# Performance work log

Measured on AMD Instinct MI355X. Metric: run time of the kernel, lower is better.

## Reference

```python
import jax, jax.numpy as jnp
import numpy as np

N = 50000   # nodes
E = 800000  # edges (before self loops)
D = 128     # hidden_channels (= input_dim here)
G = 64      # graphs in batch
NEG_SLOPE = 0.2


def setup_inputs() -> dict:
    key = jax.random.key(0)
    ks = jax.random.split(key, 16)
    s = 1.0 / np.sqrt(D)
    inp = {
        "x": jax.random.normal(ks[0], (N, D), jnp.float32),
        "edge_index": jax.random.randint(ks[1], (2, E), 0, N, dtype=jnp.int32),
        "batch": jnp.sort(jax.random.randint(ks[2], (N,), 0, G, dtype=jnp.int32)),
        "lin_in_w": jax.random.normal(ks[3], (D, D), jnp.float32) * s,
        "lin_in_b": jnp.zeros((D,), jnp.float32),
        "w1": jax.random.normal(ks[4], (D, D), jnp.float32) * s,
        "asrc1": jax.random.normal(ks[5], (D,), jnp.float32) * s,
        "adst1": jax.random.normal(ks[6], (D,), jnp.float32) * s,
        "b1": jnp.zeros((D,), jnp.float32),
        "w2": jax.random.normal(ks[7], (D, D), jnp.float32) * s,
        "asrc2": jax.random.normal(ks[8], (D,), jnp.float32) * s,
        "adst2": jax.random.normal(ks[9], (D,), jnp.float32) * s,
        "b2": jnp.zeros((D,), jnp.float32),
        "out_w": jax.random.normal(ks[10], (D, 1), jnp.float32) * s,
        "out_b": jnp.zeros((1,), jnp.float32),
    }
    return inp


def gat_conv(h_in, src, dst, W, a_src, a_dst, b):
    # h: [N, D] projected features (heads=1, concat irrelevant)
    h = h_in @ W
    alpha_s = (h * a_src).sum(-1)  # [N]
    alpha_d = (h * a_dst).sum(-1)  # [N]
    e = jax.nn.leaky_relu(alpha_s[src] + alpha_d[dst], NEG_SLOPE)  # [E+N]
    # segment softmax over destination nodes
    m = jax.ops.segment_max(e, dst, num_segments=N)
    e = jnp.exp(e - m[dst])
    denom = jax.ops.segment_sum(e, dst, num_segments=N)
    alpha = e / denom[dst]
    out = jax.ops.segment_sum(alpha[:, None] * h[src], dst, num_segments=N)
    return out + b


def reference(x, edge_index, batch, lin_in_w, lin_in_b,
              w1, asrc1, adst1, b1, w2, asrc2, adst2, b2, out_w, out_b):
    loops = jnp.arange(N, dtype=edge_index.dtype)
    src = jnp.concatenate([edge_index[0], loops])  # add_self_loops=True
    dst = jnp.concatenate([edge_index[1], loops])
    h = x @ lin_in_w + lin_in_b
    h = jax.nn.relu(gat_conv(h, src, dst, w1, asrc1, adst1, b1))
    h = jax.nn.relu(gat_conv(h, src, dst, w2, asrc2, adst2, b2))
    # global mean pool over graphs
    cnt = jax.ops.segment_sum(jnp.ones((N,), h.dtype), batch, num_segments=G)
    pooled = jax.ops.segment_sum(h, batch, num_segments=G) / cnt[:, None]
    return pooled @ out_w + out_b
```

## Files before the change

### kernel.cpp

```cpp
#include <hip/hip_runtime.h>
#include <hip/hip_bf16.h>

#define NEG_SLOPE 0.2f
#define BSHIFT 8
#define MAXBUCK 256
#define ECAP 8192
#define LDA 136

typedef __attribute__((ext_vector_type(8))) short bfrag;
typedef __attribute__((ext_vector_type(4))) float ffrag;

static __device__ __forceinline__ float b2f(unsigned short u){
  return __uint_as_float(((unsigned int)u) << 16);
}
static __device__ __forceinline__ unsigned short f2b16(float f){
  unsigned int u = __float_as_uint(f);
  return (unsigned short)((u + 0x7fffu + ((u >> 16) & 1u)) >> 16);
}
static __device__ __forceinline__ unsigned int pack_bf2(float a, float b){
  return (unsigned int)f2b16(a) | ((unsigned int)f2b16(b) << 16);
}

__global__ __launch_bounds__(256) void k_setup(const float* __restrict__ lin_w,
    const float* __restrict__ lin_b, const float* __restrict__ w1,
    const float* __restrict__ w2, unsigned short* __restrict__ Wtc,
    float* __restrict__ bc, unsigned short* __restrict__ Wt2,
    const int* __restrict__ batch, int* __restrict__ bcur,
    int* __restrict__ gs, int* __restrict__ ge, int n){
  __shared__ float Wl[64 * 128];
  __shared__ float Al[32 * 128];
  const int t = threadIdx.x;
  if(blockIdx.x >= 6){
    int i = (blockIdx.x - 6) * 256 + t;
    if(i < MAXBUCK) bcur[i] = 0;
    if(i < n){
      int g = batch[i];
      if(i == 0){
        gs[g] = 0;
      } else {
        int gp = batch[i - 1];
        if(gp != g){ gs[g] = i; ge[gp] = i; }
      }
      if(i == n - 1) ge[g] = n;
    }
    return;
  }
  if(blockIdx.x == 4){
    if(t < 128){
      float s = 0.f;
      for(int k = 0; k < 128; k++) s += lin_b[k] * w1[k * 128 + t];
      bc[t] = s;
    }
    return;
  }
  if(blockIdx.x == 5){
    #pragma unroll
    for(int i = 0; i < 16; i++){
      int idx = t + i * 256;
      int k = idx >> 5, n0 = (idx & 31) * 4;
      float4 v = ((const float4*)w2)[idx];
      Wt2[(n0+0) * 128 + k] = f2b16(v.x);
      Wt2[(n0+1) * 128 + k] = f2b16(v.y);
      Wt2[(n0+2) * 128 + k] = f2b16(v.z);
      Wt2[(n0+3) * 128 + k] = f2b16(v.w);
    }
    return;
  }
  const int row0 = blockIdx.x * 32;
  #pragma unroll
  for(int i = 0; i < 8; i++){
    int idx = t + i * 256;
    int r = idx >> 6, kk = idx & 63;
    ((float2*)Al)[r * 64 + kk] = ((const float2*)lin_w)[(size_t)(row0 + r) * 64 + kk];
  }
  const int c0 = (t & 31) * 4;
  const int rb = (t >> 5) * 4;
  float acc[4][4] = {};
  const float4* W4 = (const float4*)w1;
  #pragma unroll
  for(int h = 0; h < 2; h++){
    if(h) __syncthreads();
    #pragma unroll
    for(int i = 0; i < 8; i++) ((float4*)Wl)[t + i * 256] = W4[h * 2048 + t + i * 256];
    __syncthreads();
    const int kb = h * 64;
    #pragma unroll 8
    for(int k = 0; k < 64; k++){
      float4 wv = *(const float4*)&Wl[k * 128 + c0];
      float a0 = Al[(rb+0)*128 + kb + k];
      float a1 = Al[(rb+1)*128 + kb + k];
      float a2 = Al[(rb+2)*128 + kb + k];
      float a3 = Al[(rb+3)*128 + kb + k];
      acc[0][0] += a0*wv.x; acc[0][1] += a0*wv.y; acc[0][2] += a0*wv.z; acc[0][3] += a0*wv.w;
      acc[1][0] += a1*wv.x; acc[1][1] += a1*wv.y; acc[1][2] += a1*wv.z; acc[1][3] += a1*wv.w;
      acc[2][0] += a2*wv.x; acc[2][1] += a2*wv.y; acc[2][2] += a2*wv.z; acc[2][3] += a2*wv.w;
      acc[3][0] += a3*wv.x; acc[3][1] += a3*wv.y; acc[3][2] += a3*wv.z; acc[3][3] += a3*wv.w;
    }
  }
  #pragma unroll
  for(int j = 0; j < 4; j++){
    int rg = row0 + rb + j;
    Wtc[(c0+0) * 128 + rg] = f2b16(acc[j][0]);
    Wtc[(c0+1) * 128 + rg] = f2b16(acc[j][1]);
    Wtc[(c0+2) * 128 + rg] = f2b16(acc[j][2]);
    Wtc[(c0+3) * 128 + rg] = f2b16(acc[j][3]);
  }
}

template<bool ABF>
__global__ __launch_bounds__(256) void k_gemm_proj(const void* __restrict__ Av,
    const unsigned short* __restrict__ W, const float* __restrict__ a_src,
    const float* __restrict__ a_dst, const float* __restrict__ bias,
    unsigned int* __restrict__ hb,
    float* __restrict__ alpha_s, float* __restrict__ alpha_d, int nrows){
  __shared__ unsigned short Wt[128 * LDA];
  __shared__ unsigned short Aw[64 * LDA];
  const int t = threadIdx.x;
  const int row0 = blockIdx.x * 64;
  {
    const uint4* Wv = (const uint4*)W;
    #pragma unroll
    for(int i = 0; i < 8; i++){
      int idx = t + i * 256;
      int nr = idx >> 4, c8 = idx & 15;
      *(uint4*)&Wt[nr * LDA + c8 * 8] = Wv[idx];
    }
  }
  if(ABF){
    #pragma unroll
    for(int i = 0; i < 8; i++){
      int idx = t + i * 256;
      int r = idx >> 5;
      int rg = row0 + r; if(rg >= nrows) rg = nrows - 1;
      uint2 v = ((const uint2*)Av)[(size_t)rg * 32 + (idx & 31)];
      unsigned int* dst = (unsigned int*)&Aw[r * LDA];
      dst[(idx & 31) * 2]     = v.x;
      dst[(idx & 31) * 2 + 1] = v.y;
    }
  } else {
    #pragma unroll
    for(int i = 0; i < 16; i++){
      int idx = t + i * 256;
      int r = idx >> 6, c2 = idx & 63;
      int rg = row0 + r; if(rg >= nrows) rg = nrows - 1;
      float2 v = ((const float2*)Av)[(size_t)rg * 64 + c2];
      ((unsigned int*)&Aw[r * LDA])[c2] = pack_bf2(v.x, v.y);
    }
  }
  __syncthreads();

  const int lane = t & 63;
  const int wv = t >> 6;
  const int quad = lane >> 4, l = lane & 15;
  const int rw = wv * 16;
  bfrag a[4];
  #pragma unroll
  for(int kk = 0; kk < 4; kk++)
    a[kk] = *(const bfrag*)&Aw[(rw + l) * LDA + kk * 32 + quad * 8];
  ffrag acc[8];
  #pragma unroll
  for(int c = 0; c < 8; c++){
    ffrag z; z[0] = 0.f; z[1] = 0.f; z[2] = 0.f; z[3] = 0.f;
    acc[c] = z;
    #pragma unroll
    for(int kk = 0; kk < 4; kk++){
      bfrag b = *(const bfrag*)&Wt[(c * 16 + l) * LDA + kk * 32 + quad * 8];
      acc[c] = __builtin_amdgcn_mfma_f32_16x16x32_bf16(a[kk], b, acc[c], 0, 0, 0);
    }
  }
  float sdot[4] = {0.f,0.f,0.f,0.f}, ddot[4] = {0.f,0.f,0.f,0.f};
  #pragma unroll
  for(int c = 0; c < 8; c++){
    int col = c * 16 + l;
    float bv = bias ? bias[col] : 0.f;
    float as_ = a_src[col], ad_ = a_dst[col];
    #pragma unroll
    for(int r = 0; r < 4; r++){
      float v = acc[c][r] + bv;
      acc[c][r] = v;
      sdot[r] += v * as_;
      ddot[r] += v * ad_;
    }
  }
  #pragma unroll
  for(int r = 0; r < 4; r++){
    #pragma unroll
    for(int o = 1; o < 16; o <<= 1){
      sdot[r] += __shfl_xor(sdot[r], o);
      ddot[r] += __shfl_xor(ddot[r], o);
    }
  }
  if(l == 0){
    #pragma unroll
    for(int r = 0; r < 4; r++){
      int R = row0 + rw + quad * 4 + r;
      if(R < nrows){ alpha_s[R] = sdot[r]; alpha_d[R] = ddot[r]; }
    }
  }
  __syncthreads();
  unsigned short* ost = (unsigned short*)Aw;
  #pragma unroll
  for(int c = 0; c < 8; c++){
    int col = c * 16 + l;
    #pragma unroll
    for(int r = 0; r < 4; r++)
      ost[(rw + quad * 4 + r) * 128 + col] = f2b16(acc[c][r]);
  }
  __syncthreads();
  #pragma unroll
  for(int i = 0; i < 4; i++){
    int idx = t + i * 256;
    int r = idx >> 4;
    int rg = row0 + r;
    if(rg < nrows){
      uint4 v = ((const uint4*)ost)[idx];
      ((uint4*)&hb[(size_t)rg * 64])[idx & 15] = v;
    }
  }
}

__global__ __launch_bounds__(256) void k_binA(const int* __restrict__ ei,
    int* __restrict__ bcur, uint2* __restrict__ staged, int E, int Etot){
  __shared__ int hist[MAXBUCK];
  __shared__ int scanb[MAXBUCK];
  __shared__ int delta[MAXBUCK];
  __shared__ uint2 buf[4096];
  const int t = threadIdx.x;
  const int base = blockIdx.x * 4096;
  if(t < MAXBUCK) hist[t] = 0;
  __syncthreads();
  int myb[16], myi[16]; uint2 mye[16];
  #pragma unroll
  for(int k = 0; k < 16; k++){
    int e = base + t + k * 256;
    myb[k] = -1;
    if(e < Etot){
      int src, dst;
      if(e < E){ src = ei[e]; dst = ei[E + e]; }
      else { src = e - E; dst = src; }
      int b = dst >> BSHIFT;
      myi[k] = atomicAdd(&hist[b], 1);
      myb[k] = b;
      mye[k] = make_uint2((unsigned)src, (unsigned)dst);
    }
  }
  __syncthreads();
  if(t < MAXBUCK) scanb[t] = hist[t];
  __syncthreads();
  for(int off = 1; off < MAXBUCK; off <<= 1){
    int v = (t < MAXBUCK && t >= off) ? scanb[t - off] : 0;
    __syncthreads();
    if(t < MAXBUCK) scanb[t] += v;
    __syncthreads();
  }
  if(t < MAXBUCK){
    int excl = scanb[t] - hist[t];
    int gb = (hist[t] > 0) ? atomicAdd(&bcur[t], hist[t]) : 0;
    delta[t] = t * ECAP + gb - excl;
    scanb[t] = excl;
  }
  __syncthreads();
  #pragma unroll
  for(int k = 0; k < 16; k++){
    if(myb[k] >= 0) buf[scanb[myb[k]] + myi[k]] = mye[k];
  }
  __syncthreads();
  int total = min(4096, Etot - base);
  for(int i = t; i < total; i += 256){
    uint2 ed = buf[i];
    int b = (int)(ed.y >> BSHIFT);
    staged[i + delta[b]] = ed;
  }
}

__global__ __launch_bounds__(256) void k_binB(const uint2* __restrict__ staged,
    const int* __restrict__ bcur, int* __restrict__ rowptr, int* __restrict__ esrc, int n){
  __shared__ int sc[MAXBUCK];
  __shared__ int dcnt[1 << BSHIFT];
  __shared__ int doff[1 << BSHIFT];
  const int b = blockIdx.x;
  const int n0 = b << BSHIFT;
  const int t = threadIdx.x;
  int cv = bcur[t];
  sc[t] = cv;
  __syncthreads();
  for(int off = 1; off < MAXBUCK; off <<= 1){
    int x = (t >= off) ? sc[t - off] : 0;
    __syncthreads();
    sc[t] += x;
    __syncthreads();
  }
  const int cnt = bcur[b];
  const int lo = sc[b] - cnt;
  if(t == 0 && b == (int)gridDim.x - 1) rowptr[n] = sc[MAXBUCK - 1];
  const uint2* run = staged + (size_t)b * ECAP;
  dcnt[t] = 0;
  __syncthreads();
  for(int j = t; j < cnt; j += 256){
    uint2 ed = run[j];
    atomicAdd(&dcnt[(int)(ed.y) - n0], 1);
  }
  __syncthreads();
  int v = dcnt[t];
  doff[t] = v;
  __syncthreads();
  for(int off = 1; off < (1 << BSHIFT); off <<= 1){
    int x = (t >= off) ? doff[t - off] : 0;
    __syncthreads();
    doff[t] += x;
    __syncthreads();
  }
  int excl = doff[t] - v;
  int i = n0 + t;
  if(i < n) rowptr[i] = lo + excl;
  dcnt[t] = excl;
  __syncthreads();
  for(int j = t; j < cnt; j += 256){
    uint2 ed = run[j];
    int pos = atomicAdd(&dcnt[(int)(ed.y) - n0], 1);
    esrc[lo + pos] = (int)ed.x;
  }
}

static __device__ __forceinline__ void gat_fullwave(const unsigned int* __restrict__ hb,
    const int* __restrict__ esrc, const float* __restrict__ a_s,
    const float* __restrict__ a_d, const float* __restrict__ bias,
    unsigned int* __restrict__ hb_out, uint2* pairs_w,
    int w, int s0, int s1, int lane, int n){
  const int deg = s1 - s0;
  const float adv = a_d[w];
  float2 acc0 = make_float2(0.f, 0.f), acc1 = make_float2(0.f, 0.f);
  float2 acc2 = make_float2(0.f, 0.f), acc3 = make_float2(0.f, 0.f);
  if(deg <= 64){
    int srcl = 0;
    if(lane < deg){
      srcl = esrc[s0 + lane];
      srcl = ((unsigned)srcl < (unsigned)n) ? srcl : 0;
    }
    int i0 = __shfl(srcl, 0), i1 = __shfl(srcl, 1);
    int i2 = __shfl(srcl, 2), i3 = __shfl(srcl, 3);
    int i4 = __shfl(srcl, 4), i5 = __shfl(srcl, 5);
    int i6 = __shfl(srcl, 6), i7 = __shfl(srcl, 7);
    unsigned int u0 = hb[(((unsigned)i0) << 6) + lane];
    unsigned int u1 = hb[(((unsigned)i1) << 6) + lane];
    unsigned int u2 = hb[(((unsigned)i2) << 6) + lane];
    unsigned int u3 = hb[(((unsigned)i3) << 6) + lane];
    unsigned int u4 = hb[(((unsigned)i4) << 6) + lane];
    unsigned int u5 = hb[(((unsigned)i5) << 6) + lane];
    unsigned int u6 = hb[(((unsigned)i6) << 6) + lane];
    unsigned int u7 = hb[(((unsigned)i7) << 6) + lane];
    float e = -1e30f;
    if(lane < deg){
      float v = a_s[srcl] + adv;
      e = v > 0.f ? v : NEG_SLOPE * v;
    }
    float m = e;
    #pragma unroll
    for(int o = 32; o; o >>= 1) m = fmaxf(m, __shfl_xor(m, o));
    float wgt = (lane < deg) ? __expf(e - m) : 0.f;
    float den = wgt;
    #pragma unroll
    for(int o = 32; o; o >>= 1) den += __shfl_xor(den, o);
    float winv = (den > 0.f) ? wgt / den : 0.f;
    pairs_w[lane] = make_uint2((unsigned)srcl, __float_as_uint(winv));
    float w0 = __shfl(winv, 0), w1 = __shfl(winv, 1);
    float w2 = __shfl(winv, 2), w3 = __shfl(winv, 3);
    float w4 = __shfl(winv, 4), w5 = __shfl(winv, 5);
    float w6 = __shfl(winv, 6), w7 = __shfl(winv, 7);
    acc0.x += w0 * b2f((unsigned short)(u0 & 0xffffu)); acc0.y += w0 * b2f((unsigned short)(u0 >> 16));
    acc1.x += w1 * b2f((unsigned short)(u1 & 0xffffu)); acc1.y += w1 * b2f((unsigned short)(u1 >> 16));
    acc2.x += w2 * b2f((unsigned short)(u2 & 0xffffu)); acc2.y += w2 * b2f((unsigned short)(u2 >> 16));
    acc3.x += w3 * b2f((unsigned short)(u3 & 0xffffu)); acc3.y += w3 * b2f((unsigned short)(u3 >> 16));
    acc0.x += w4 * b2f((unsigned short)(u4 & 0xffffu)); acc0.y += w4 * b2f((unsigned short)(u4 >> 16));
    acc1.x += w5 * b2f((unsigned short)(u5 & 0xffffu)); acc1.y += w5 * b2f((unsigned short)(u5 >> 16));
    acc2.x += w6 * b2f((unsigned short)(u6 & 0xffffu)); acc2.y += w6 * b2f((unsigned short)(u6 >> 16));
    acc3.x += w7 * b2f((unsigned short)(u7 & 0xffffu)); acc3.y += w7 * b2f((unsigned short)(u7 >> 16));
    int jj = 8;
    for(; jj + 8 <= deg; jj += 8){
      uint2 p0 = pairs_w[jj + 0], p1 = pairs_w[jj + 1];
      uint2 p2 = pairs_w[jj + 2], p3 = pairs_w[jj + 3];
      uint2 p4 = pairs_w[jj + 4], p5 = pairs_w[jj + 5];
      uint2 p6 = pairs_w[jj + 6], p7 = pairs_w[jj + 7];
      unsigned int v0 = hb[(p0.x << 6) + lane];
      unsigned int v1 = hb[(p1.x << 6) + lane];
      unsigned int v2 = hb[(p2.x << 6) + lane];
      unsigned int v3 = hb[(p3.x << 6) + lane];
      unsigned int v4 = hb[(p4.x << 6) + lane];
      unsigned int v5 = hb[(p5.x << 6) + lane];
      unsigned int v6 = hb[(p6.x << 6) + lane];
      unsigned int v7 = hb[(p7.x << 6) + lane];
      float q0 = __uint_as_float(p0.y), q1 = __uint_as_float(p1.y);
      float q2 = __uint_as_float(p2.y), q3 = __uint_as_float(p3.y);
      float q4 = __uint_as_float(p4.y), q5 = __uint_as_float(p5.y);
      float q6 = __uint_as_float(p6.y), q7 = __uint_as_float(p7.y);
      acc0.x += q0 * b2f((unsigned short)(v0 & 0xffffu)); acc0.y += q0 * b2f((unsigned short)(v0 >> 16));
      acc1.x += q1 * b2f((unsigned short)(v1 & 0xffffu)); acc1.y += q1 * b2f((unsigned short)(v1 >> 16));
      acc2.x += q2 * b2f((unsigned short)(v2 & 0xffffu)); acc2.y += q2 * b2f((unsigned short)(v2 >> 16));
      acc3.x += q3 * b2f((unsigned short)(v3 & 0xffffu)); acc3.y += q3 * b2f((unsigned short)(v3 >> 16));
      acc0.x += q4 * b2f((unsigned short)(v4 & 0xffffu)); acc0.y += q4 * b2f((unsigned short)(v4 >> 16));
      acc1.x += q5 * b2f((unsigned short)(v5 & 0xffffu)); acc1.y += q5 * b2f((unsigned short)(v5 >> 16));
      acc2.x += q6 * b2f((unsigned short)(v6 & 0xffffu)); acc2.y += q6 * b2f((unsigned short)(v6 >> 16));
      acc3.x += q7 * b2f((unsigned short)(v7 & 0xffffu)); acc3.y += q7 * b2f((unsigned short)(v7 >> 16));
    }
    for(; jj < deg; jj++){
      uint2 p = pairs_w[jj];
      unsigned int v = hb[(p.x << 6) + lane];
      float q = __uint_as_float(p.y);
      acc0.x += q * b2f((unsigned short)(v & 0xffffu));
      acc0.y += q * b2f((unsigned short)(v >> 16));
    }
  } else {
    float m = -1e30f;
    for(int j = s0 + lane; j < s1; j += 64){
      int s = esrc[j]; s = ((unsigned)s < (unsigned)n) ? s : 0;
      float e = a_s[s] + adv;
      e = e > 0.f ? e : NEG_SLOPE * e;
      m = fmaxf(m, e);
    }
    #pragma unroll
    for(int o = 32; o; o >>= 1) m = fmaxf(m, __shfl_xor(m, o));
    float den = 0.f;
    for(int j = s0 + lane; j < s1; j += 64){
      int s = esrc[j]; s = ((unsigned)s < (unsigned)n) ? s : 0;
      float e = a_s[s] + adv;
      e = e > 0.f ? e : NEG_SLOPE * e;
      den += __expf(e - m);
    }
    #pragma unroll
    for(int o = 32; o; o >>= 1) den += __shfl_xor(den, o);
    float inv = (den > 0.f) ? 1.f / den : 0.f;
    for(int j = s0; j < s1; j++){
      int s = esrc[j]; s = ((unsigned)s < (unsigned)n) ? s : 0;
      float e = a_s[s] + adv;
      e = e > 0.f ? e : NEG_SLOPE * e;
      float wv = __expf(e - m) * inv;
      unsigned int u = hb[(((unsigned)s) << 6) + lane];
      acc0.x += wv * b2f((unsigned short)(u & 0xffffu));
      acc0.y += wv * b2f((unsigned short)(u >> 16));
    }
  }
  float2 bl = ((const float2*)bias)[lane];
  float ox = (acc0.x + acc1.x) + (acc2.x + acc3.x) + bl.x;
  float oy = (acc0.y + acc1.y) + (acc2.y + acc3.y) + bl.y;
  ox = 0.5f * (ox + fabsf(ox));
  oy = 0.5f * (oy + fabsf(oy));
  hb_out[(size_t)w * 64 + lane] = pack_bf2(ox, oy);
}

__global__ __launch_bounds__(256) void k_gat(const unsigned int* __restrict__ hb,
    const int* __restrict__ rowptr, const int* __restrict__ esrc,
    const float* __restrict__ a_s, const float* __restrict__ a_d,
    const float* __restrict__ bias, unsigned int* __restrict__ hb_out, int n, int Etot){
  __shared__ uint2 pairs[4][64];
  const int t = threadIdx.x;
  const int lane = t & 63;
  const int wvid = t >> 6;
  const int nA = blockIdx.x * 8 + wvid * 2;
  if(nA >= n) return;
  const int nB = nA + 1;
  int r0 = rowptr[nA];
  int r1 = rowptr[nA + 1];
  int r2 = (nB < n) ? rowptr[nB + 1] : r1;
  r0 = max(0, min(r0, Etot));
  r1 = max(r0, min(r1, Etot));
  r2 = max(r1, min(r2, Etot));
  const int degA = r1 - r0, degB = r2 - r1;

  if(degA <= 32 && degB <= 32){
    const int half = lane >> 5;
    const int hl = lane & 31;
    const int w = nA + half;
    const int s0 = half ? r1 : r0;
    const int deg = half ? degB : degA;
    const float adv = (w < n) ? a_d[w] : 0.f;
    const uint2* hb2v = (const uint2*)hb;
    float4 accA = make_float4(0.f, 0.f, 0.f, 0.f);
    float4 accB = make_float4(0.f, 0.f, 0.f, 0.f);

    int srcl = 0;
    if(hl < deg){
      srcl = esrc[s0 + hl];
      srcl = ((unsigned)srcl < (unsigned)n) ? srcl : 0;
    }
    const int hb0 = lane & 32;
    int i0 = __shfl(srcl, hb0 + 0), i1 = __shfl(srcl, hb0 + 1);
    int i2 = __shfl(srcl, hb0 + 2), i3 = __shfl(srcl, hb0 + 3);
    int i4 = __shfl(srcl, hb0 + 4), i5 = __shfl(srcl, hb0 + 5);
    int i6 = __shfl(srcl, hb0 + 6), i7 = __shfl(srcl, hb0 + 7);
    uint2 u0 = hb2v[(((unsigned)i0) << 5) + hl];
    uint2 u1 = hb2v[(((unsigned)i1) << 5) + hl];
    uint2 u2 = hb2v[(((unsigned)i2) << 5) + hl];
    uint2 u3 = hb2v[(((unsigned)i3) << 5) + hl];
    uint2 u4 = hb2v[(((unsigned)i4) << 5) + hl];
    uint2 u5 = hb2v[(((unsigned)i5) << 5) + hl];
    uint2 u6 = hb2v[(((unsigned)i6) << 5) + hl];
    uint2 u7 = hb2v[(((unsigned)i7) << 5) + hl];
    float e = -1e30f;
    if(hl < deg){
      float v = a_s[srcl] + adv;
      e = v > 0.f ? v : NEG_SLOPE * v;
    }
    float m = e;
    #pragma unroll
    for(int o = 16; o; o >>= 1) m = fmaxf(m, __shfl_xor(m, o));
    float wgt = (hl < deg) ? __expf(e - m) : 0.f;
    float den = wgt;
    #pragma unroll
    for(int o = 16; o; o >>= 1) den += __shfl_xor(den, o);
    float winv = (den > 0.f) ? wgt / den : 0.f;
    pairs[wvid][lane] = make_uint2((unsigned)srcl, __float_as_uint(winv));
    float w0 = __shfl(winv, hb0 + 0), w1 = __shfl(winv, hb0 + 1);
    float w2 = __shfl(winv, hb0 + 2), w3 = __shfl(winv, hb0 + 3);
    float w4 = __shfl(winv, hb0 + 4), w5 = __shfl(winv, hb0 + 5);
    float w6 = __shfl(winv, hb0 + 6), w7 = __shfl(winv, hb0 + 7);
    accA.x += w0 * b2f((unsigned short)(u0.x & 0xffffu)); accA.y += w0 * b2f((unsigned short)(u0.x >> 16));
    accA.z += w0 * b2f((unsigned short)(u0.y & 0xffffu)); accA.w += w0 * b2f((unsigned short)(u0.y >> 16));
    accB.x += w1 * b2f((unsigned short)(u1.x & 0xffffu)); accB.y += w1 * b2f((unsigned short)(u1.x >> 16));
    accB.z += w1 * b2f((unsigned short)(u1.y & 0xffffu)); accB.w += w1 * b2f((unsigned short)(u1.y >> 16));
    accA.x += w2 * b2f((unsigned short)(u2.x & 0xffffu)); accA.y += w2 * b2f((unsigned short)(u2.x >> 16));
    accA.z += w2 * b2f((unsigned short)(u2.y & 0xffffu)); accA.w += w2 * b2f((unsigned short)(u2.y >> 16));
    accB.x += w3 * b2f((unsigned short)(u3.x & 0xffffu)); accB.y += w3 * b2f((unsigned short)(u3.x >> 16));
    accB.z += w3 * b2f((unsigned short)(u3.y & 0xffffu)); accB.w += w3 * b2f((unsigned short)(u3.y >> 16));
    accA.x += w4 * b2f((unsigned short)(u4.x & 0xffffu)); accA.y += w4 * b2f((unsigned short)(u4.x >> 16));
    accA.z += w4 * b2f((unsigned short)(u4.y & 0xffffu)); accA.w += w4 * b2f((unsigned short)(u4.y >> 16));
    accB.x += w5 * b2f((unsigned short)(u5.x & 0xffffu)); accB.y += w5 * b2f((unsigned short)(u5.x >> 16));
    accB.z += w5 * b2f((unsigned short)(u5.y & 0xffffu)); accB.w += w5 * b2f((unsigned short)(u5.y >> 16));
    accA.x += w6 * b2f((unsigned short)(u6.x & 0xffffu)); accA.y += w6 * b2f((unsigned short)(u6.x >> 16));
    accA.z += w6 * b2f((unsigned short)(u6.y & 0xffffu)); accA.w += w6 * b2f((unsigned short)(u6.y >> 16));
    accB.x += w7 * b2f((unsigned short)(u7.x & 0xffffu)); accB.y += w7 * b2f((unsigned short)(u7.x >> 16));
    accB.z += w7 * b2f((unsigned short)(u7.y & 0xffffu)); accB.w += w7 * b2f((unsigned short)(u7.y >> 16));
    int jj = 8;
    for(; jj + 8 <= deg; jj += 8){
      uint2 p0 = pairs[wvid][hb0 + jj + 0], p1 = pairs[wvid][hb0 + jj + 1];
      uint2 p2 = pairs[wvid][hb0 + jj + 2], p3 = pairs[wvid][hb0 + jj + 3];
      uint2 p4 = pairs[wvid][hb0 + jj + 4], p5 = pairs[wvid][hb0 + jj + 5];
      uint2 p6 = pairs[wvid][hb0 + jj + 6], p7 = pairs[wvid][hb0 + jj + 7];
      uint2 v0 = hb2v[(p0.x << 5) + hl];
      uint2 v1 = hb2v[(p1.x << 5) + hl];
      uint2 v2 = hb2v[(p2.x << 5) + hl];
      uint2 v3 = hb2v[(p3.x << 5) + hl];
      uint2 v4 = hb2v[(p4.x << 5) + hl];
      uint2 v5 = hb2v[(p5.x << 5) + hl];
      uint2 v6 = hb2v[(p6.x << 5) + hl];
      uint2 v7 = hb2v[(p7.x << 5) + hl];
      float q0 = __uint_as_float(p0.y), q1 = __uint_as_float(p1.y);
      float q2 = __uint_as_float(p2.y), q3 = __uint_as_float(p3.y);
      float q4 = __uint_as_float(p4.y), q5 = __uint_as_float(p5.y);
      float q6 = __uint_as_float(p6.y), q7 = __uint_as_float(p7.y);
      accA.x += q0 * b2f((unsigned short)(v0.x & 0xffffu)); accA.y += q0 * b2f((unsigned short)(v0.x >> 16));
      accA.z += q0 * b2f((unsigned short)(v0.y & 0xffffu)); accA.w += q0 * b2f((unsigned short)(v0.y >> 16));
      accB.x += q1 * b2f((unsigned short)(v1.x & 0xffffu)); accB.y += q1 * b2f((unsigned short)(v1.x >> 16));
      accB.z += q1 * b2f((unsigned short)(v1.y & 0xffffu)); accB.w += q1 * b2f((unsigned short)(v1.y >> 16));
      accA.x += q2 * b2f((unsigned short)(v2.x & 0xffffu)); accA.y += q2 * b2f((unsigned short)(v2.x >> 16));
      accA.z += q2 * b2f((unsigned short)(v2.y & 0xffffu)); accA.w += q2 * b2f((unsigned short)(v2.y >> 16));
      accB.x += q3 * b2f((unsigned short)(v3.x & 0xffffu)); accB.y += q3 * b2f((unsigned short)(v3.x >> 16));
      accB.z += q3 * b2f((unsigned short)(v3.y & 0xffffu)); accB.w += q3 * b2f((unsigned short)(v3.y >> 16));
      accA.x += q4 * b2f((unsigned short)(v4.x & 0xffffu)); accA.y += q4 * b2f((unsigned short)(v4.x >> 16));
      accA.z += q4 * b2f((unsigned short)(v4.y & 0xffffu)); accA.w += q4 * b2f((unsigned short)(v4.y >> 16));
      accB.x += q5 * b2f((unsigned short)(v5.x & 0xffffu)); accB.y += q5 * b2f((unsigned short)(v5.x >> 16));
      accB.z += q5 * b2f((unsigned short)(v5.y & 0xffffu)); accB.w += q5 * b2f((unsigned short)(v5.y >> 16));
      accA.x += q6 * b2f((unsigned short)(v6.x & 0xffffu)); accA.y += q6 * b2f((unsigned short)(v6.x >> 16));
      accA.z += q6 * b2f((unsigned short)(v6.y & 0xffffu)); accA.w += q6 * b2f((unsigned short)(v6.y >> 16));
      accB.x += q7 * b2f((unsigned short)(v7.x & 0xffffu)); accB.y += q7 * b2f((unsigned short)(v7.x >> 16));
      accB.z += q7 * b2f((unsigned short)(v7.y & 0xffffu)); accB.w += q7 * b2f((unsigned short)(v7.y >> 16));
    }
    if(jj + 4 <= deg){
      uint2 p0 = pairs[wvid][hb0 + jj + 0], p1 = pairs[wvid][hb0 + jj + 1];
      uint2 p2 = pairs[wvid][hb0 + jj + 2], p3 = pairs[wvid][hb0 + jj + 3];
      uint2 v0 = hb2v[(p0.x << 5) + hl];
      uint2 v1 = hb2v[(p1.x << 5) + hl];
      uint2 v2 = hb2v[(p2.x << 5) + hl];
      uint2 v3 = hb2v[(p3.x << 5) + hl];
      float q0 = __uint_as_float(p0.y), q1 = __uint_as_float(p1.y);
      float q2 = __uint_as_float(p2.y), q3 = __uint_as_float(p3.y);
      accA.x += q0 * b2f((unsigned short)(v0.x & 0xffffu)); accA.y += q0 * b2f((unsigned short)(v0.x >> 16));
      accA.z += q0 * b2f((unsigned short)(v0.y & 0xffffu)); accA.w += q0 * b2f((unsigned short)(v0.y >> 16));
      accB.x += q1 * b2f((unsigned short)(v1.x & 0xffffu)); accB.y += q1 * b2f((unsigned short)(v1.x >> 16));
      accB.z += q1 * b2f((unsigned short)(v1.y & 0xffffu)); accB.w += q1 * b2f((unsigned short)(v1.y >> 16));
      accA.x += q2 * b2f((unsigned short)(v2.x & 0xffffu)); accA.y += q2 * b2f((unsigned short)(v2.x >> 16));
      accA.z += q2 * b2f((unsigned short)(v2.y & 0xffffu)); accA.w += q2 * b2f((unsigned short)(v2.y >> 16));
      accB.x += q3 * b2f((unsigned short)(v3.x & 0xffffu)); accB.y += q3 * b2f((unsigned short)(v3.x >> 16));
      accB.z += q3 * b2f((unsigned short)(v3.y & 0xffffu)); accB.w += q3 * b2f((unsigned short)(v3.y >> 16));
      jj += 4;
    }
    for(; jj < deg; jj++){
      uint2 p = pairs[wvid][hb0 + jj];
      uint2 v = hb2v[(p.x << 5) + hl];
      float q = __uint_as_float(p.y);
      accA.x += q * b2f((unsigned short)(v.x & 0xffffu)); accA.y += q * b2f((unsigned short)(v.x >> 16));
      accA.z += q * b2f((unsigned short)(v.y & 0xffffu)); accA.w += q * b2f((unsigned short)(v.y >> 16));
    }
    if(w < n){
      float4 bl = ((const float4*)bias)[hl];
      float f0 = accA.x + accB.x + bl.x;
      float f1 = accA.y + accB.y + bl.y;
      float f2 = accA.z + accB.z + bl.z;
      float f3 = accA.w + accB.w + bl.w;
      f0 = 0.5f * (f0 + fabsf(f0));
      f1 = 0.5f * (f1 + fabsf(f1));
      f2 = 0.5f * (f2 + fabsf(f2));
      f3 = 0.5f * (f3 + fabsf(f3));
      ((uint2*)hb_out)[((size_t)w << 5) + hl] = make_uint2(pack_bf2(f0, f1), pack_bf2(f2, f3));
    }
  } else {
    gat_fullwave(hb, esrc, a_s, a_d, bias, hb_out, &pairs[wvid][0], nA, r0, r1, lane, n);
    if(nB < n)
      gat_fullwave(hb, esrc, a_s, a_d, bias, hb_out, &pairs[wvid][0], nB, r1, r2, lane, n);
  }
}

__global__ __launch_bounds__(512) void k_poolout(const unsigned int* __restrict__ h2,
    const int* __restrict__ gs, const int* __restrict__ ge,
    const float* __restrict__ out_w, const float* __restrict__ out_b,
    float* __restrict__ out, int n){
  const int g = blockIdx.x;
  const int t = threadIdx.x;
  const int f2 = t & 63;
  const int rr = t >> 6;
  int s = gs[g], e = ge[g];
  s = max(0, min(s, n)); e = max(s, min(e, n));
  float sx = 0.f, sy = 0.f;
  for(int i = s + rr; i < e; i += 8){
    unsigned int u = h2[(size_t)i * 64 + f2];
    sx += b2f((unsigned short)(u & 0xffffu));
    sy += b2f((unsigned short)(u >> 16));
  }
  __shared__ float part[8 * 128];
  part[rr * 128 + 2 * f2]     = sx;
  part[rr * 128 + 2 * f2 + 1] = sy;
  __syncthreads();
  __shared__ float red[2];
  if(t < 128){
    float tot = 0.f;
    #pragma unroll
    for(int r = 0; r < 8; r++) tot += part[r * 128 + t];
    int c = e - s;
    float invc = (c > 0) ? 1.f / (float)c : 0.f;
    float v = tot * invc * out_w[t];
    #pragma unroll
    for(int o = 32; o; o >>= 1) v += __shfl_xor(v, o);
    if((t & 63) == 0) red[t >> 6] = v;
  }
  __syncthreads();
  if(t == 0) out[g] = red[0] + red[1] + out_b[0];
}

extern "C" void kernel_launch(void* const* d_in, const int* in_sizes, int n_in,
                              void* d_out, int out_size, void* d_ws, size_t ws_size,
                              hipStream_t stream){
  const float* x     = (const float*)d_in[0];
  const int*   ei    = (const int*)d_in[1];
  const int*   batch = (const int*)d_in[2];
  const float* lin_w = (const float*)d_in[3];
  const float* lin_b = (const float*)d_in[4];
  const float* w1    = (const float*)d_in[5];
  const float* as1   = (const float*)d_in[6];
  const float* ad1   = (const float*)d_in[7];
  const float* b1    = (const float*)d_in[8];
  const float* w2    = (const float*)d_in[9];
  const float* as2   = (const float*)d_in[10];
  const float* ad2   = (const float*)d_in[11];
  const float* b2    = (const float*)d_in[12];
  const float* ow    = (const float*)d_in[13];
  const float* ob    = (const float*)d_in[14];
  float* out = (float*)d_out;

  const int N = in_sizes[0] / 128;
  const int E = in_sizes[1] / 2;
  const int Etot = E + N;
  const int G = out_size;
  const int nbuck = (N + (1 << BSHIFT) - 1) >> BSHIFT;

  auto a16 = [](size_t v){ return (v + 15) & ~(size_t)15; };
  char* p = (char*)d_ws;
  int*   rowptr  = (int*)p;   p += a16((size_t)(N + 1) * 4);
  int*   bcur    = (int*)p;   p += a16((size_t)MAXBUCK * 4);
  int*   gs      = (int*)p;   p += a16((size_t)G * 4);
  int*   ge      = (int*)p;   p += a16((size_t)G * 4);
  float* alpha_s = (float*)p; p += a16((size_t)N * 4);
  float* alpha_d = (float*)p; p += a16((size_t)N * 4);
  unsigned short* Wtc = (unsigned short*)p; p += (size_t)128 * 128 * 2;
  float* bc      = (float*)p; p += (size_t)128 * 4;
  unsigned short* Wt2 = (unsigned short*)p; p += (size_t)128 * 128 * 2;
  int*   esrc    = (int*)p;   p += a16((size_t)Etot * 4);
  uint2* staged  = (uint2*)p; p += (size_t)MAXBUCK * ECAP * 8;
  unsigned int* hb  = (unsigned int*)p; p += (size_t)N * 64 * 4;
  unsigned int* hb2 = (unsigned int*)p; p += (size_t)N * 64 * 4;

  const int cbl = (Etot + 4095) / 4096;
  k_setup<<<6 + (N + 255) / 256, 256, 0, stream>>>(lin_w, lin_b, w1, w2, Wtc, bc, Wt2,
                                                   batch, bcur, gs, ge, N);
  k_binA<<<cbl, 256, 0, stream>>>(ei, bcur, staged, E, Etot);
  k_binB<<<nbuck, 256, 0, stream>>>(staged, bcur, rowptr, esrc, N);

  const int gbl = (N + 63) / 64;
  const int wbl = (N + 7) / 8;

  k_gemm_proj<false><<<gbl, 256, 0, stream>>>(x, Wtc, as1, ad1, bc, hb, alpha_s, alpha_d, N);
  k_gat<<<wbl, 256, 0, stream>>>(hb, rowptr, esrc, alpha_s, alpha_d, b1, hb2, N, Etot);
  k_gemm_proj<true><<<gbl, 256, 0, stream>>>(hb2, Wt2, as2, ad2, nullptr, hb, alpha_s, alpha_d, N);
  k_gat<<<wbl, 256, 0, stream>>>(hb, rowptr, esrc, alpha_s, alpha_d, b2, hb2, N, Etot);
  k_poolout<<<G, 512, 0, stream>>>(hb2, gs, ge, ow, ob, out, N);
}
```

Before: 261.7 us.

## Fuse first projection GEMM with edge binning, widen GAT gathers to 16B

```diff
diff --git a/kernel.cpp b/kernel.cpp
--- a/kernel.cpp
+++ b/kernel.cpp
@@ -6,6 +6,7 @@
 #define MAXBUCK 256
 #define ECAP 8192
 #define LDA 136
+#define SMEM_BYTES 52224
 
 typedef __attribute__((ext_vector_type(8))) short bfrag;
 typedef __attribute__((ext_vector_type(4))) float ffrag;
@@ -108,15 +109,15 @@
 }
 
 template<bool ABF>
-__global__ __launch_bounds__(256) void k_gemm_proj(const void* __restrict__ Av,
+static __device__ __forceinline__ void gemm_body(uint4* smem, const void* __restrict__ Av,
     const unsigned short* __restrict__ W, const float* __restrict__ a_src,
     const float* __restrict__ a_dst, const float* __restrict__ bias,
     unsigned int* __restrict__ hb,
-    float* __restrict__ alpha_s, float* __restrict__ alpha_d, int nrows){
-  __shared__ unsigned short Wt[128 * LDA];
-  __shared__ unsigned short Aw[64 * LDA];
+    float* __restrict__ alpha_s, float* __restrict__ alpha_d, int nrows, int blk){
+  unsigned short* Wt = (unsigned short*)smem;
+  unsigned short* Aw = Wt + 128 * LDA;
   const int t = threadIdx.x;
-  const int row0 = blockIdx.x * 64;
+  const int row0 = blk * 64;
   {
     const uint4* Wv = (const uint4*)W;
     #pragma unroll
@@ -198,7 +199,7 @@
     }
   }
   __syncthreads();
-  unsigned short* ost = (unsigned short*)Aw;
+  unsigned short* ost = Aw;
   #pragma unroll
   for(int c = 0; c < 8; c++){
     int col = c * 16 + l;
@@ -219,14 +220,14 @@
   }
 }
 
-__global__ __launch_bounds__(256) void k_binA(const int* __restrict__ ei,
-    int* __restrict__ bcur, uint2* __restrict__ staged, int E, int Etot){
-  __shared__ int hist[MAXBUCK];
-  __shared__ int scanb[MAXBUCK];
-  __shared__ int delta[MAXBUCK];
-  __shared__ uint2 buf[4096];
+static __device__ __forceinline__ void binA_body(uint4* smem, const int* __restrict__ ei,
+    int* __restrict__ bcur, uint2* __restrict__ staged, int E, int Etot, int blk){
+  int* hist  = (int*)smem;
+  int* scanb = hist + MAXBUCK;
+  int* delta = scanb + MAXBUCK;
+  uint2* buf = (uint2*)(delta + MAXBUCK);
   const int t = threadIdx.x;
-  const int base = blockIdx.x * 4096;
+  const int base = blk * 4096;
   if(t < MAXBUCK) hist[t] = 0;
   __syncthreads();
   int myb[16], myi[16]; uint2 mye[16];
@@ -271,6 +272,29 @@
     int b = (int)(ed.y >> BSHIFT);
     staged[i + delta[b]] = ed;
   }
+}
+
+__global__ __launch_bounds__(256) void k_gemm1_binA(const void* __restrict__ Av,
+    const unsigned short* __restrict__ W, const float* __restrict__ a_src,
+    const float* __restrict__ a_dst, const float* __restrict__ bias,
+    unsigned int* __restrict__ hb, float* __restrict__ alpha_s, float* __restrict__ alpha_d,
+    int nrows, const int* __restrict__ ei, int* __restrict__ bcur,
+    uint2* __restrict__ staged, int E, int Etot, int gbl){
+  extern __shared__ uint4 smem_dyn[];
+  if((int)blockIdx.x < gbl)
+    gemm_body<false>(smem_dyn, Av, W, a_src, a_dst, bias, hb, alpha_s, alpha_d, nrows,
+                     (int)blockIdx.x);
+  else
+    binA_body(smem_dyn, ei, bcur, staged, E, Etot, (int)blockIdx.x - gbl);
+}
+
+__global__ __launch_bounds__(256) void k_gemm2(const void* __restrict__ Av,
+    const unsigned short* __restrict__ W, const float* __restrict__ a_src,
+    const float* __restrict__ a_dst, unsigned int* __restrict__ hb,
+    float* __restrict__ alpha_s, float* __restrict__ alpha_d, int nrows){
+  __shared__ uint4 smem_s[SMEM_BYTES / 16];
+  gemm_body<true>(smem_s, Av, W, a_src, a_dst, nullptr, hb, alpha_s, alpha_d, nrows,
+                  (int)blockIdx.x);
 }
 
 __global__ __launch_bounds__(256) void k_binB(const uint2* __restrict__ staged,
@@ -447,6 +471,16 @@
   hb_out[(size_t)w * 64 + lane] = pack_bf2(ox, oy);
 }
 
+#define ACC8(U, WQ) do{ float _w = (WQ); \
+  acc0.x += _w * b2f((unsigned short)((U).x & 0xffffu)); \
+  acc0.y += _w * b2f((unsigned short)((U).x >> 16)); \
+  acc0.z += _w * b2f((unsigned short)((U).y & 0xffffu)); \
+  acc0.w += _w * b2f((unsigned short)((U).y >> 16)); \
+  acc1.x += _w * b2f((unsigned short)((U).z & 0xffffu)); \
+  acc1.y += _w * b2f((unsigned short)((U).z >> 16)); \
+  acc1.z += _w * b2f((unsigned short)((U).w & 0xffffu)); \
+  acc1.w += _w * b2f((unsigned short)((U).w >> 16)); }while(0)
+
 __global__ __launch_bounds__(256) void k_gat(const unsigned int* __restrict__ hb,
     const int* __restrict__ rowptr, const int* __restrict__ esrc,
     const float* __restrict__ a_s, const float* __restrict__ a_d,
@@ -469,13 +503,15 @@
   if(degA <= 32 && degB <= 32){
     const int half = lane >> 5;
     const int hl = lane & 31;
+    const int sub = hl >> 4;
+    const int fl = hl & 15;
     const int w = nA + half;
     const int s0 = half ? r1 : r0;
     const int deg = half ? degB : degA;
     const float adv = (w < n) ? a_d[w] : 0.f;
-    const uint2* hb2v = (const uint2*)hb;
-    float4 accA = make_float4(0.f, 0.f, 0.f, 0.f);
-    float4 accB = make_float4(0.f, 0.f, 0.f, 0.f);
+    const uint4* __restrict__ hb4 = (const uint4*)hb;
+    float4 acc0 = make_float4(0.f, 0.f, 0.f, 0.f);
+    float4 acc1 = make_float4(0.f, 0.f, 0.f, 0.f);
 
     int srcl = 0;
     if(hl < deg){
@@ -483,18 +519,22 @@
       srcl = ((unsigned)srcl < (unsigned)n) ? srcl : 0;
     }
     const int hb0 = lane & 32;
-    int i0 = __shfl(srcl, hb0 + 0), i1 = __shfl(srcl, hb0 + 1);
-    int i2 = __shfl(srcl, hb0 + 2), i3 = __shfl(srcl, hb0 + 3);
-    int i4 = __shfl(srcl, hb0 + 4), i5 = __shfl(srcl, hb0 + 5);
-    int i6 = __shfl(srcl, hb0 + 6), i7 = __shfl(srcl, hb0 + 7);
-    uint2 u0 = hb2v[(((unsigned)i0) << 5) + hl];
-    uint2 u1 = hb2v[(((unsigned)i1) << 5) + hl];
-    uint2 u2 = hb2v[(((unsigned)i2) << 5) + hl];
-    uint2 u3 = hb2v[(((unsigned)i3) << 5) + hl];
-    uint2 u4 = hb2v[(((unsigned)i4) << 5) + hl];
-    uint2 u5 = hb2v[(((unsigned)i5) << 5) + hl];
-    uint2 u6 = hb2v[(((unsigned)i6) << 5) + hl];
-    uint2 u7 = hb2v[(((unsigned)i7) << 5) + hl];
+    int e0 = __shfl(srcl, hb0 + 0  + sub);
+    int e1 = __shfl(srcl, hb0 + 2  + sub);
+    int e2 = __shfl(srcl, hb0 + 4  + sub);
+    int e3 = __shfl(srcl, hb0 + 6  + sub);
+    int e4 = __shfl(srcl, hb0 + 8  + sub);
+    int e5 = __shfl(srcl, hb0 + 10 + sub);
+    int e6 = __shfl(srcl, hb0 + 12 + sub);
+    int e7 = __shfl(srcl, hb0 + 14 + sub);
+    uint4 u0 = hb4[(((unsigned)e0) << 4) + fl];
+    uint4 u1 = hb4[(((unsigned)e1) << 4) + fl];
+    uint4 u2 = hb4[(((unsigned)e2) << 4) + fl];
+    uint4 u3 = hb4[(((unsigned)e3) << 4) + fl];
+    uint4 u4 = hb4[(((unsigned)e4) << 4) + fl];
+    uint4 u5 = hb4[(((unsigned)e5) << 4) + fl];
+    uint4 u6 = hb4[(((unsigned)e6) << 4) + fl];
+    uint4 u7 = hb4[(((unsigned)e7) << 4) + fl];
     float e = -1e30f;
     if(hl < deg){
       float v = a_s[srcl] + adv;
@@ -509,98 +549,55 @@
     for(int o = 16; o; o >>= 1) den += __shfl_xor(den, o);
     float winv = (den > 0.f) ? wgt / den : 0.f;
     pairs[wvid][lane] = make_uint2((unsigned)srcl, __float_as_uint(winv));
-    float w0 = __shfl(winv, hb0 + 0), w1 = __shfl(winv, hb0 + 1);
-    float w2 = __shfl(winv, hb0 + 2), w3 = __shfl(winv, hb0 + 3);
-    float w4 = __shfl(winv, hb0 + 4), w5 = __shfl(winv, hb0 + 5);
-    float w6 = __shfl(winv, hb0 + 6), w7 = __shfl(winv, hb0 + 7);
-    accA.x += w0 * b2f((unsigned short)(u0.x & 0xffffu)); accA.y += w0 * b2f((unsigned short)(u0.x >> 16));
-    accA.z += w0 * b2f((unsigned short)(u0.y & 0xffffu)); accA.w += w0 * b2f((unsigned short)(u0.y >> 16));
-    accB.x += w1 * b2f((unsigned short)(u1.x & 0xffffu)); accB.y += w1 * b2f((unsigned short)(u1.x >> 16));
-    accB.z += w1 * b2f((unsigned short)(u1.y & 0xffffu)); accB.w += w1 * b2f((unsigned short)(u1.y >> 16));
-    accA.x += w2 * b2f((unsigned short)(u2.x & 0xffffu)); accA.y += w2 * b2f((unsigned short)(u2.x >> 16));
-    accA.z += w2 * b2f((unsigned short)(u2.y & 0xffffu)); accA.w += w2 * b2f((unsigned short)(u2.y >> 16));
-    accB.x += w3 * b2f((unsigned short)(u3.x & 0xffffu)); accB.y += w3 * b2f((unsigned short)(u3.x >> 16));
-    accB.z += w3 * b2f((unsigned short)(u3.y & 0xffffu)); accB.w += w3 * b2f((unsigned short)(u3.y >> 16));
-    accA.x += w4 * b2f((unsigned short)(u4.x & 0xffffu)); accA.y += w4 * b2f((unsigned short)(u4.x >> 16));
-    accA.z += w4 * b2f((unsigned short)(u4.y & 0xffffu)); accA.w += w4 * b2f((unsigned short)(u4.y >> 16));
-    accB.x += w5 * b2f((unsigned short)(u5.x & 0xffffu)); accB.y += w5 * b2f((unsigned short)(u5.x >> 16));
-    accB.z += w5 * b2f((unsigned short)(u5.y & 0xffffu)); accB.w += w5 * b2f((unsigned short)(u5.y >> 16));
-    accA.x += w6 * b2f((unsigned short)(u6.x & 0xffffu)); accA.y += w6 * b2f((unsigned short)(u6.x >> 16));
-    accA.z += w6 * b2f((unsigned short)(u6.y & 0xffffu)); accA.w += w6 * b2f((unsigned short)(u6.y >> 16));
-    accB.x += w7 * b2f((unsigned short)(u7.x & 0xffffu)); accB.y += w7 * b2f((unsigned short)(u7.x >> 16));
-    accB.z += w7 * b2f((unsigned short)(u7.y & 0xffffu)); accB.w += w7 * b2f((unsigned short)(u7.y >> 16));
-    int jj = 8;
-    for(; jj + 8 <= deg; jj += 8){
-      uint2 p0 = pairs[wvid][hb0 + jj + 0], p1 = pairs[wvid][hb0 + jj + 1];
-      uint2 p2 = pairs[wvid][hb0 + jj + 2], p3 = pairs[wvid][hb0 + jj + 3];
-      uint2 p4 = pairs[wvid][hb0 + jj + 4], p5 = pairs[wvid][hb0 + jj + 5];
-      uint2 p6 = pairs[wvid][hb0 + jj + 6], p7 = pairs[wvid][hb0 + jj + 7];
-      uint2 v0 = hb2v[(p0.x << 5) + hl];
-      uint2 v1 = hb2v[(p1.x << 5) + hl];
-      uint2 v2 = hb2v[(p2.x << 5) + hl];
-      uint2 v3 = hb2v[(p3.x << 5) + hl];
-      uint2 v4 = hb2v[(p4.x << 5) + hl];
-      uint2 v5 = hb2v[(p5.x << 5) + hl];
-      uint2 v6 = hb2v[(p6.x << 5) + hl];
-      uint2 v7 = hb2v[(p7.x << 5) + hl];
-      float q0 = __uint_as_float(p0.y), q1 = __uint_as_float(p1.y);
-      float q2 = __uint_as_float(p2.y), q3 = __uint_as_float(p3.y);
-      float q4 = __uint_as_float(p4.y), q5 = __uint_as_float(p5.y);
-      float q6 = __uint_as_float(p6.y), q7 = __uint_as_float(p7.y);
-      accA.x += q0 * b2f((unsigned short)(v0.x & 0xffffu)); accA.y += q0 * b2f((unsigned short)(v0.x >> 16));
-      accA.z += q0 * b2f((unsigned short)(v0.y & 0xffffu)); accA.w += q0 * b2f((unsigned short)(v0.y >> 16));
-      accB.x += q1 * b2f((unsigned short)(v1.x & 0xffffu)); accB.y += q1 * b2f((unsigned short)(v1.x >> 16));
-      accB.z += q1 * b2f((unsigned short)(v1.y & 0xffffu)); accB.w += q1 * b2f((unsigned short)(v1.y >> 16));
-      accA.x += q2 * b2f((unsigned short)(v2.x & 0xffffu)); accA.y += q2 * b2f((unsigned short)(v2.x >> 16));
-      accA.z += q2 * b2f((unsigned short)(v2.y & 0xffffu)); accA.w += q2 * b2f((unsigned short)(v2.y >> 16));
-      accB.x += q3 * b2f((unsigned short)(v3.x & 0xffffu)); accB.y += q3 * b2f((unsigned short)(v3.x >> 16));
-      accB.z += q3 * b2f((unsigned short)(v3.y & 0xffffu)); accB.w += q3 * b2f((unsigned short)(v3.y >> 16));
-      accA.x += q4 * b2f((unsigned short)(v4.x & 0xffffu)); accA.y += q4 * b2f((unsigned short)(v4.x >> 16));
-      accA.z += q4 * b2f((unsigned short)(v4.y & 0xffffu)); accA.w += q4 * b2f((unsigned short)(v4.y >> 16));
-      accB.x += q5 * b2f((unsigned short)(v5.x & 0xffffu)); accB.y += q5 * b2f((unsigned short)(v5.x >> 16));
-      accB.z += q5 * b2f((unsigned short)(v5.y & 0xffffu)); accB.w += q5 * b2f((unsigned short)(v5.y >> 16));
-      accA.x += q6 * b2f((unsigned short)(v6.x & 0xffffu)); accA.y += q6 * b2f((unsigned short)(v6.x >> 16));
-      accA.z += q6 * b2f((unsigned short)(v6.y & 0xffffu)); accA.w += q6 * b2f((unsigned short)(v6.y >> 16));
-      accB.x += q7 * b2f((unsigned short)(v7.x & 0xffffu)); accB.y += q7 * b2f((unsigned short)(v7.x >> 16));
-      accB.z += q7 * b2f((unsigned short)(v7.y & 0xffffu)); accB.w += q7 * b2f((unsigned short)(v7.y >> 16));
-    }
-    if(jj + 4 <= deg){
-      uint2 p0 = pairs[wvid][hb0 + jj + 0], p1 = pairs[wvid][hb0 + jj + 1];
-      uint2 p2 = pairs[wvid][hb0 + jj + 2], p3 = pairs[wvid][hb0 + jj + 3];
-      uint2 v0 = hb2v[(p0.x << 5) + hl];
-      uint2 v1 = hb2v[(p1.x << 5) + hl];
-      uint2 v2 = hb2v[(p2.x << 5) + hl];
-      uint2 v3 = hb2v[(p3.x << 5) + hl];
-      float q0 = __uint_as_float(p0.y), q1 = __uint_as_float(p1.y);
-      float q2 = __uint_as_float(p2.y), q3 = __uint_as_float(p3.y);
-      accA.x += q0 * b2f((unsigned short)(v0.x & 0xffffu)); accA.y += q0 * b2f((unsigned short)(v0.x >> 16));
-      accA.z += q0 * b2f((unsigned short)(v0.y & 0xffffu)); accA.w += q0 * b2f((unsigned short)(v0.y >> 16));
-      accB.x += q1 * b2f((unsigned short)(v1.x & 0xffffu)); accB.y += q1 * b2f((unsigned short)(v1.x >> 16));
-      accB.z += q1 * b2f((unsigned short)(v1.y & 0xffffu)); accB.w += q1 * b2f((unsigned short)(v1.y >> 16));
-      accA.x += q2 * b2f((unsigned short)(v2.x & 0xffffu)); accA.y += q2 * b2f((unsigned short)(v2.x >> 16));
-      accA.z += q2 * b2f((unsigned short)(v2.y & 0xffffu)); accA.w += q2 * b2f((unsigned short)(v2.y >> 16));
-      accB.x += q3 * b2f((unsigned short)(v3.x & 0xffffu)); accB.y += q3 * b2f((unsigned short)(v3.x >> 16));
-      accB.z += q3 * b2f((unsigned short)(v3.y & 0xffffu)); accB.w += q3 * b2f((unsigned short)(v3.y >> 16));
-      jj += 4;
-    }
-    for(; jj < deg; jj++){
-      uint2 p = pairs[wvid][hb0 + jj];
-      uint2 v = hb2v[(p.x << 5) + hl];
-      float q = __uint_as_float(p.y);
-      accA.x += q * b2f((unsigned short)(v.x & 0xffffu)); accA.y += q * b2f((unsigned short)(v.x >> 16));
-      accA.z += q * b2f((unsigned short)(v.y & 0xffffu)); accA.w += q * b2f((unsigned short)(v.y >> 16));
-    }
-    if(w < n){
-      float4 bl = ((const float4*)bias)[hl];
-      float f0 = accA.x + accB.x + bl.x;
-      float f1 = accA.y + accB.y + bl.y;
-      float f2 = accA.z + accB.z + bl.z;
-      float f3 = accA.w + accB.w + bl.w;
-      f0 = 0.5f * (f0 + fabsf(f0));
-      f1 = 0.5f * (f1 + fabsf(f1));
-      f2 = 0.5f * (f2 + fabsf(f2));
-      f3 = 0.5f * (f3 + fabsf(f3));
-      ((uint2*)hb_out)[((size_t)w << 5) + hl] = make_uint2(pack_bf2(f0, f1), pack_bf2(f2, f3));
+    float w0 = __shfl(winv, hb0 + 0  + sub);
+    float w1 = __shfl(winv, hb0 + 2  + sub);
+    float w2 = __shfl(winv, hb0 + 4  + sub);
+    float w3 = __shfl(winv, hb0 + 6  + sub);
+    float w4 = __shfl(winv, hb0 + 8  + sub);
+    float w5 = __shfl(winv, hb0 + 10 + sub);
+    float w6 = __shfl(winv, hb0 + 12 + sub);
+    float w7 = __shfl(winv, hb0 + 14 + sub);
+    ACC8(u0, w0); ACC8(u1, w1); ACC8(u2, w2); ACC8(u3, w3);
+    ACC8(u4, w4); ACC8(u5, w5); ACC8(u6, w6); ACC8(u7, w7);
+    if(deg > 16){
+      uint2 p0 = pairs[wvid][hb0 + 16 + sub];
+      uint2 p1 = pairs[wvid][hb0 + 18 + sub];
+      uint2 p2 = pairs[wvid][hb0 + 20 + sub];
+      uint2 p3 = pairs[wvid][hb0 + 22 + sub];
+      uint2 p4 = pairs[wvid][hb0 + 24 + sub];
+      uint2 p5 = pairs[wvid][hb0 + 26 + sub];
+      uint2 p6 = pairs[wvid][hb0 + 28 + sub];
+      uint2 p7 = pairs[wvid][hb0 + 30 + sub];
+      uint4 v0 = hb4[(p0.x << 4) + fl];
+      uint4 v1 = hb4[(p1.x << 4) + fl];
+      uint4 v2 = hb4[(p2.x << 4) + fl];
+      uint4 v3 = hb4[(p3.x << 4) + fl];
+      uint4 v4 = hb4[(p4.x << 4) + fl];
+      uint4 v5 = hb4[(p5.x << 4) + fl];
+      uint4 v6 = hb4[(p6.x << 4) + fl];
+      uint4 v7 = hb4[(p7.x << 4) + fl];
+      ACC8(v0, __uint_as_float(p0.y)); ACC8(v1, __uint_as_float(p1.y));
+      ACC8(v2, __uint_as_float(p2.y)); ACC8(v3, __uint_as_float(p3.y));
+      ACC8(v4, __uint_as_float(p4.y)); ACC8(v5, __uint_as_float(p5.y));
+      ACC8(v6, __uint_as_float(p6.y)); ACC8(v7, __uint_as_float(p7.y));
+    }
+    acc0.x += __shfl_xor(acc0.x, 16); acc0.y += __shfl_xor(acc0.y, 16);
+    acc0.z += __shfl_xor(acc0.z, 16); acc0.w += __shfl_xor(acc0.w, 16);
+    acc1.x += __shfl_xor(acc1.x, 16); acc1.y += __shfl_xor(acc1.y, 16);
+    acc1.z += __shfl_xor(acc1.z, 16); acc1.w += __shfl_xor(acc1.w, 16);
+    if(w < n && sub == 0){
+      float4 b0 = ((const float4*)bias)[2 * fl];
+      float4 b1 = ((const float4*)bias)[2 * fl + 1];
+      float f0 = acc0.x + b0.x, f1 = acc0.y + b0.y;
+      float f2 = acc0.z + b0.z, f3 = acc0.w + b0.w;
+      float f4 = acc1.x + b1.x, f5 = acc1.y + b1.y;
+      float f6 = acc1.z + b1.z, f7 = acc1.w + b1.w;
+      f0 = 0.5f * (f0 + fabsf(f0)); f1 = 0.5f * (f1 + fabsf(f1));
+      f2 = 0.5f * (f2 + fabsf(f2)); f3 = 0.5f * (f3 + fabsf(f3));
+      f4 = 0.5f * (f4 + fabsf(f4)); f5 = 0.5f * (f5 + fabsf(f5));
+      f6 = 0.5f * (f6 + fabsf(f6)); f7 = 0.5f * (f7 + fabsf(f7));
+      ((uint4*)hb_out)[((size_t)w << 4) + fl] =
+        make_uint4(pack_bf2(f0, f1), pack_bf2(f2, f3), pack_bf2(f4, f5), pack_bf2(f6, f7));
     }
   } else {
     gat_fullwave(hb, esrc, a_s, a_d, bias, hb_out, &pairs[wvid][0], nA, r0, r1, lane, n);
@@ -688,17 +685,17 @@
   unsigned int* hb2 = (unsigned int*)p; p += (size_t)N * 64 * 4;
 
   const int cbl = (Etot + 4095) / 4096;
+  const int gbl = (N + 63) / 64;
+  const int wbl = (N + 7) / 8;
+
   k_setup<<<6 + (N + 255) / 256, 256, 0, stream>>>(lin_w, lin_b, w1, w2, Wtc, bc, Wt2,
                                                    batch, bcur, gs, ge, N);
-  k_binA<<<cbl, 256, 0, stream>>>(ei, bcur, staged, E, Etot);
+  k_gemm1_binA<<<gbl + cbl, 256, SMEM_BYTES, stream>>>(x, Wtc, as1, ad1, bc, hb,
+                                                       alpha_s, alpha_d, N,
+                                                       ei, bcur, staged, E, Etot, gbl);
   k_binB<<<nbuck, 256, 0, stream>>>(staged, bcur, rowptr, esrc, N);
-
-  const int gbl = (N + 63) / 64;
-  const int wbl = (N + 7) / 8;
-
-  k_gemm_proj<false><<<gbl, 256, 0, stream>>>(x, Wtc, as1, ad1, bc, hb, alpha_s, alpha_d, N);
   k_gat<<<wbl, 256, 0, stream>>>(hb, rowptr, esrc, alpha_s, alpha_d, b1, hb2, N, Etot);
-  k_gemm_proj<true><<<gbl, 256, 0, stream>>>(hb2, Wt2, as2, ad2, nullptr, hb, alpha_s, alpha_d, N);
+  k_gemm2<<<gbl, 256, 0, stream>>>(hb2, Wt2, as2, ad2, hb, alpha_s, alpha_d, N);
   k_gat<<<wbl, 256, 0, stream>>>(hb, rowptr, esrc, alpha_s, alpha_d, b2, hb2, N, Etot);
   k_poolout<<<G, 512, 0, stream>>>(hb2, gs, ge, ow, ob, out, N);
 }
```

After: 259.0 us. No clear change (-1.0%).
